# Kernel optimization log

Hardware: AMD Instinct MI355X
Metric: run time of the kernel (lower is better)

The kernel has to match this reference:

```python
import jax, jax.numpy as jnp
import numpy as np

B, C, L = 32, 64, 2048
FREQ = L // 2 + 1            # 1025
BAND_SIZES = [341, 341, 343]  # freq//3, freq//3, remainder


def setup_inputs() -> dict:
    key = jax.random.key(0)
    k = jax.random.split(key, 6)
    X = jax.random.normal(k[0], (B, C, L), dtype=jnp.float32)
    A0 = jax.random.normal(k[1], (BAND_SIZES[0], BAND_SIZES[0]), dtype=jnp.float32)
    A1 = jax.random.normal(k[2], (BAND_SIZES[1], BAND_SIZES[1]), dtype=jnp.float32)
    A2 = jax.random.normal(k[3], (BAND_SIZES[2], BAND_SIZES[2]), dtype=jnp.float32)
    fusion_weights = jnp.ones((3,), dtype=jnp.float32)
    # Gumbel(0,1) noise for the 2-way gumbel-softmax over each (b, i, j) entry
    gumbel_noise = jax.random.gumbel(k[4], (B, C, C, 2), dtype=jnp.float32)
    return {"X": X, "A0": A0, "A1": A1, "A2": A2,
            "fusion_weights": fusion_weights, "gumbel_noise": gumbel_noise}


def _band_dist(band, A):
    # band: (b, c, s), A: (s, s). dist[b,i,j] = ||A (band_i - band_j)||^2
    # Gram trick: ||y_i - y_j||^2 = q_i + q_j - 2 y_i . y_j, y = band @ A^T
    Y = jnp.einsum('ds,bcs->bcd', A, band)          # (b, c, s)
    G = jnp.einsum('bid,bjd->bij', Y, Y)            # (b, c, c)
    q = jnp.einsum('bid,bid->bi', Y, Y)             # (b, c)
    dist = q[:, :, None] + q[:, None, :] - 2.0 * G
    return jnp.maximum(dist, 0.0)                   # guard fp round-off


def reference(X, A0, A1, A2, fusion_weights, gumbel_noise):
    XF = jnp.abs(jnp.fft.rfft(X, axis=-1))          # (b, c, FREQ)
    s0, s1, s2 = BAND_SIZES
    bands = (XF[..., :s0], XF[..., s0:s0 + s1], XF[..., s0 + s1:])
    As = (A0, A1, A2)
    dists = jnp.stack([_band_dist(b_, A_) for b_, A_ in zip(bands, As)], axis=-1)  # (b,c,c,3)
    w = jax.nn.softmax(fusion_weights)
    dist = jnp.einsum('bijk,k->bij', dists, w)      # (b, c, c)

    exp_dist = 1.0 / (dist + 1e-10)
    eye = jnp.eye(C, dtype=exp_dist.dtype)
    mask = 1.0 - eye
    exp_dist = exp_dist * mask
    exp_max = jax.lax.stop_gradient(jnp.max(exp_dist, axis=-1, keepdims=True))
    p = exp_dist / exp_max
    p = (p * mask + eye) * 0.99                     # probs in (0, 0.99]

    # Bernoulli via 2-class gumbel-softmax (hard, tau=1, straight-through)
    logits = jnp.stack([jnp.log(p / (1.0 - p)), jnp.log((1.0 - p) / p)], axis=-1)  # (b,c,c,2)
    y = logits + gumbel_noise
    y_soft = jax.nn.softmax(y, axis=-1)
    y_hard = jax.nn.one_hot(jnp.argmax(y, axis=-1), 2, dtype=y_soft.dtype)
    sample = (y_hard - jax.lax.stop_gradient(y_soft) + y_soft)[..., 0]  # (b,c,c)
    return sample[:, None, :, :]                    # (b, 1, c, c)
```

## Files before the change

kernel.cpp:

```cpp
#include <hip/hip_runtime.h>
#include <math.h>

#define Bn 32
#define Cn 64
#define Ln 2048
#define NFREQ 1025
#define S0c 341
#define S1c 341
#define S2c 343

#define PI_D 3.14159265358979323846

typedef double v4d __attribute__((ext_vector_type(4)));
typedef unsigned short u16;
typedef __attribute__((ext_vector_type(4))) u16 u16x4;
typedef __attribute__((ext_vector_type(8))) short short8;
typedef __attribute__((ext_vector_type(4))) float f32x4;

#define PADIX(i) ((i) + ((i) >> 4))

__device__ __forceinline__ u16 rneb(float f) {
    unsigned u = __float_as_uint(f);
    unsigned r = (u + 0x7FFFu + ((u >> 16) & 1u)) >> 16;
    return (u16)r;
}
__device__ __forceinline__ float b2f(u16 h) {
    return __uint_as_float(((unsigned)h) << 16);
}
__device__ __forceinline__ void split3(float v, u16& h1, u16& h2, u16& h3) {
    h1 = rneb(v);
    float r1 = v - b2f(h1);
    h2 = rneb(r1);
    float r2 = r1 - b2f(h2);
    h3 = rneb(r2);
}

__global__ void k_twiddle(double2* __restrict__ tw) {
    int t = blockIdx.x * blockDim.x + threadIdx.x;
    if (t < 2048) {
        double ang = -2.0 * PI_D * (double)t / 2048.0;
        double s, c;
        sincos(ang, &s, &c);
        tw[t] = make_double2(c, s);
    }
}

__device__ __forceinline__ int rev4_10(unsigned x) {
    unsigned t = __brev(x) >> 22;
    return (int)(((t & 0x155u) << 1) | ((t >> 1) & 0x155u));
}

__global__ __launch_bounds__(256) void k_fft(const float* __restrict__ X,
                                             const double2* __restrict__ tw,
                                             float* __restrict__ XF) {
    __shared__ double re[1088];
    __shared__ double im[1088];
    int row = blockIdx.x;
    int tid = threadIdx.x;
    {
        int k = tid;
        double2 w1 = tw[2 * k];
        double2 w2 = tw[4 * k];
        double2 w3 = tw[6 * k];
        int i0 = PADIX(k), i1 = PADIX(k + 256), i2 = PADIX(k + 512), i3 = PADIX(k + 768);
        const float2* xr = (const float2*)(X + (size_t)row * Ln);
        float2 v0 = xr[k];
        float2 v1 = xr[k + 256];
        float2 v2 = xr[k + 512];
        float2 v3 = xr[k + 768];
        double ar = (double)v0.x, ai = (double)v0.y;
        double br = (double)v1.x, bi = (double)v1.y;
        double cr = (double)v2.x, ci = (double)v2.y;
        double dr = (double)v3.x, di = (double)v3.y;
        double t0r = ar + cr, t0i = ai + ci;
        double t1r = ar - cr, t1i = ai - ci;
        double t2r = br + dr, t2i = bi + di;
        double t3r = br - dr, t3i = bi - di;
        re[i0] = t0r + t2r; im[i0] = t0i + t2i;
        double u1r = t1r + t3i, u1i = t1i - t3r;
        re[i1] = u1r * w1.x - u1i * w1.y; im[i1] = u1r * w1.y + u1i * w1.x;
        double u2r = t0r - t2r, u2i = t0i - t2i;
        re[i2] = u2r * w2.x - u2i * w2.y; im[i2] = u2r * w2.y + u2i * w2.x;
        double u3r = t1r - t3i, u3i = t1i + t3r;
        re[i3] = u3r * w3.x - u3i * w3.y; im[i3] = u3r * w3.y + u3i * w3.x;
    }
    __syncthreads();
    #pragma unroll
    for (int s = 1; s < 5; ++s) {
        int log2Q = 8 - 2 * s;
        int Q = 1 << log2Q;
        int k = tid & (Q - 1);
        int g = tid >> log2Q;
        int base = (g << (log2Q + 2)) + k;
        int i0 = PADIX(base), i1 = PADIX(base + Q), i2 = PADIX(base + 2 * Q), i3 = PADIX(base + 3 * Q);
        int step = 2 << (2 * s);
        double2 w1 = tw[k * step];
        double2 w2 = tw[2 * k * step];
        double2 w3 = tw[3 * k * step];
        double ar = re[i0], ai = im[i0];
        double br = re[i1], bi = im[i1];
        double cr = re[i2], ci = im[i2];
        double dr = re[i3], di = im[i3];
        double t0r = ar + cr, t0i = ai + ci;
        double t1r = ar - cr, t1i = ai - ci;
        double t2r = br + dr, t2i = bi + di;
        double t3r = br - dr, t3i = bi - di;
        re[i0] = t0r + t2r; im[i0] = t0i + t2i;
        double u1r = t1r + t3i, u1i = t1i - t3r;
        re[i1] = u1r * w1.x - u1i * w1.y; im[i1] = u1r * w1.y + u1i * w1.x;
        double u2r = t0r - t2r, u2i = t0i - t2i;
        re[i2] = u2r * w2.x - u2i * w2.y; im[i2] = u2r * w2.y + u2i * w2.x;
        double u3r = t1r - t3i, u3i = t1i + t3r;
        re[i3] = u3r * w3.x - u3i * w3.y; im[i3] = u3r * w3.y + u3i * w3.x;
        __syncthreads();
    }
    float* out0 = XF + (size_t)row * NFREQ;
    for (int k = tid; k <= 1024; k += 256) {
        double Xr, Xi;
        if (k == 0)        { Xr = re[0] + im[0]; Xi = 0.0; }
        else if (k == 1024){ Xr = re[0] - im[0]; Xi = 0.0; }
        else {
            int rv  = PADIX(rev4_10((unsigned)k));
            int rv2 = PADIX(rev4_10((unsigned)(1024 - k)));
            double2 t = tw[k];
            double Zr = re[rv],  Zi = im[rv];
            double Wr = re[rv2], Wi = im[rv2];
            double Er = 0.5 * (Zr + Wr), Ei = 0.5 * (Zi - Wi);
            double Or = 0.5 * (Zi + Wi), Oi = -0.5 * (Zr - Wr);
            Xr = Er + t.x * Or - t.y * Oi;
            Xi = Ei + t.x * Oi + t.y * Or;
        }
        out0[k] = (float)sqrt(Xr * Xr + Xi * Xi);
    }
}

__global__ __launch_bounds__(256) void k_gemm(const float* __restrict__ XF,
                                              const float* __restrict__ A0,
                                              const float* __restrict__ A1,
                                              const float* __restrict__ A2,
                                              double* __restrict__ Y) {
    const int Sarr[3] = {S0c, S1c, S2c};
    const int Oarr[3] = {0, S0c, S0c + S1c};
    int bz = blockIdx.z;
    int z = bz >> 2, q = bz & 3;
    const float* A = (z == 0) ? A0 : ((z == 1) ? A1 : A2);
    int S = Sarr[z], O = Oarr[z];
    int qm = q >> 1, qn = q & 1;

    __shared__ u16 sX1[32][40], sX2[32][40], sX3[32][40];
    __shared__ u16 sA1[32][40], sA2[32][40], sA3[32][40];

    int r0 = blockIdx.x * 64 + qm * 32;
    int d0 = blockIdx.y * 64 + qn * 32;
    int tid = threadIdx.x;
    int lane = tid & 63, w = tid >> 6;
    int lm = (w >> 1) * 16, ln = (w & 1) * 16;
    int fm = lane & 15, kq = lane >> 4;
    int row8 = tid >> 3, seg4 = (tid & 7) * 4;

    f32x4 z4 = {0.0f, 0.0f, 0.0f, 0.0f};
    short8 aone, afm;
    {
        u16 hone = 0x3F80;
        u16 hfm = rneb((float)fm);
        #pragma unroll
        for (int j = 0; j < 8; ++j) { aone[j] = (short)hone; afm[j] = (short)hfm; }
    }
    f32x4 calR = __builtin_amdgcn_mfma_f32_16x16x32_bf16(afm, aone, z4, 0, 0, 0);
    f32x4 calC = __builtin_amdgcn_mfma_f32_16x16x32_bf16(aone, afm, z4, 0, 0, 0);
    int rIdx[4], cIdx[4];
    #pragma unroll
    for (int i = 0; i < 4; ++i) {
        rIdx[i] = (int)(calR[i] * 0.03125f + 0.5f);
        cIdx[i] = (int)(calC[i] * 0.03125f + 0.5f);
    }

    u16x4 wx1, wx2, wx3, wa1, wa2, wa3;
    auto load_tile = [&](int st) {
        int ss0 = st * 32 + seg4;
        const float* xrow = XF + (size_t)(r0 + row8) * NFREQ + O;
        int dA = d0 + row8;
        bool dv = dA < S;
        const float* arow = A + (size_t)dA * S;
        #pragma unroll
        for (int j = 0; j < 4; ++j) {
            int ss = ss0 + j;
            bool sv = ss < S;
            float xv = sv ? xrow[ss] : 0.0f;
            float av = (sv && dv) ? arow[ss] : 0.0f;
            u16 h1, h2, h3;
            split3(xv, h1, h2, h3); wx1[j] = h1; wx2[j] = h2; wx3[j] = h3;
            split3(av, h1, h2, h3); wa1[j] = h1; wa2[j] = h2; wa3[j] = h3;
        }
    };

    double accd[4] = {0.0, 0.0, 0.0, 0.0};
    load_tile(0);
    int nsteps = (S + 31) / 32;
    for (int st = 0; st < nsteps; ++st) {
        __syncthreads();
        *(u16x4*)&sX1[row8][seg4] = wx1;
        *(u16x4*)&sX2[row8][seg4] = wx2;
        *(u16x4*)&sX3[row8][seg4] = wx3;
        *(u16x4*)&sA1[row8][seg4] = wa1;
        *(u16x4*)&sA2[row8][seg4] = wa2;
        *(u16x4*)&sA3[row8][seg4] = wa3;
        __syncthreads();
        if (st + 1 < nsteps) load_tile(st + 1);
        short8 a1 = *(const short8*)&sX1[lm + fm][kq * 8];
        short8 a2 = *(const short8*)&sX2[lm + fm][kq * 8];
        short8 a3 = *(const short8*)&sX3[lm + fm][kq * 8];
        short8 b1 = *(const short8*)&sA1[ln + fm][kq * 8];
        short8 b2 = *(const short8*)&sA2[ln + fm][kq * 8];
        short8 b3 = *(const short8*)&sA3[ln + fm][kq * 8];
        f32x4 p1 = __builtin_amdgcn_mfma_f32_16x16x32_bf16(a1, b1, z4, 0, 0, 0);
        f32x4 p2 = __builtin_amdgcn_mfma_f32_16x16x32_bf16(a1, b2, z4, 0, 0, 0);
        p2 = __builtin_amdgcn_mfma_f32_16x16x32_bf16(a2, b1, p2, 0, 0, 0);
        p2 = __builtin_amdgcn_mfma_f32_16x16x32_bf16(a1, b3, p2, 0, 0, 0);
        p2 = __builtin_amdgcn_mfma_f32_16x16x32_bf16(a2, b2, p2, 0, 0, 0);
        p2 = __builtin_amdgcn_mfma_f32_16x16x32_bf16(a3, b1, p2, 0, 0, 0);
        #pragma unroll
        for (int i = 0; i < 4; ++i)
            accd[i] += (double)p1[i] + (double)p2[i];
    }
    #pragma unroll
    for (int i = 0; i < 4; ++i) {
        int row = r0 + lm + rIdx[i];
        int d = d0 + ln + cIdx[i];
        if (d < S) Y[(size_t)row * NFREQ + O + d] = accd[i];
    }
}

__global__ __launch_bounds__(256) void k_dist(const double* __restrict__ Y,
                                              const float* __restrict__ fw,
                                              double* __restrict__ part) {
    __shared__ double sY[64][34];
    int b = blockIdx.x;
    int chunk = blockIdx.y;
    int dlo = chunk * 128;
    int dhi = (chunk == 7) ? NFREQ : dlo + 128;
    int tid = threadIdx.x;
    int lane = tid & 63, w = tid >> 6;
    int wm = (w >> 1) * 32, wn = (w & 1) * 32;
    int fm = lane & 15, kq = lane >> 4;
    int kl = tid & 31, rl = tid >> 5;

    double f0 = (double)fw[0], f1 = (double)fw[1], f2 = (double)fw[2];
    double m = fmax(f0, fmax(f1, f2));
    double e0 = exp(f0 - m), e1 = exp(f1 - m), e2 = exp(f2 - m);
    double esum = e0 + e1 + e2;
    double sw0 = sqrt(e0 / esum), sw1 = sqrt(e1 / esum), sw2 = sqrt(e2 / esum);

    v4d zero = {0.0, 0.0, 0.0, 0.0};
    double aval = (double)fm;
    v4d calR = __builtin_amdgcn_mfma_f64_16x16x4f64(aval, 1.0, zero, 0, 0, 0);
    v4d calC = __builtin_amdgcn_mfma_f64_16x16x4f64(1.0, aval, zero, 0, 0, 0);
    int rIdx[4], cIdx[4];
    #pragma unroll
    for (int i = 0; i < 4; ++i) {
        rIdx[i] = (int)(calR[i] * 0.25);
        cIdx[i] = (int)(calC[i] * 0.25);
    }

    const double* Yb = Y + (size_t)b * Cn * NFREQ;
    auto load_tile = [&](int k0, double* py) {
        int d = dlo + k0 + kl;
        bool dv = d < dhi;
        double sw = dv ? ((d < S0c) ? sw0 : ((d < S0c + S1c) ? sw1 : sw2)) : 0.0;
        #pragma unroll
        for (int i = 0; i < 8; ++i)
            py[i] = dv ? Yb[(size_t)(rl + 8 * i) * NFREQ + d] * sw : 0.0;
    };

    v4d acc00 = zero, acc01 = zero, acc10 = zero, acc11 = zero;
    double py[8];
    load_tile(0, py);
    int nsteps = (dhi - dlo + 31) / 32;
    for (int st = 0; st < nsteps; ++st) {
        __syncthreads();
        #pragma unroll
        for (int i = 0; i < 8; ++i) sY[rl + 8 * i][kl] = py[i];
        __syncthreads();
        if (st + 1 < nsteps) load_tile((st + 1) * 32, py);
        #pragma unroll
        for (int t = 0; t < 8; ++t) {
            int k = 4 * t + kq;
            double a0 = sY[wm + fm][k];
            double a1 = sY[wm + 16 + fm][k];
            double b0 = sY[wn + fm][k];
            double b1 = sY[wn + 16 + fm][k];
            acc00 = __builtin_amdgcn_mfma_f64_16x16x4f64(a0, b0, acc00, 0, 0, 0);
            acc01 = __builtin_amdgcn_mfma_f64_16x16x4f64(a0, b1, acc01, 0, 0, 0);
            acc10 = __builtin_amdgcn_mfma_f64_16x16x4f64(a1, b0, acc10, 0, 0, 0);
            acc11 = __builtin_amdgcn_mfma_f64_16x16x4f64(a1, b1, acc11, 0, 0, 0);
        }
    }
    double* pb = part + (((size_t)b * 8 + chunk) << 12);
    #pragma unroll
    for (int i = 0; i < 4; ++i) {
        int rowA = wm + rIdx[i], rowB = rowA + 16;
        int cA = wn + cIdx[i], cB = cA + 16;
        pb[rowA * 64 + cA] = acc00[i];
        pb[rowA * 64 + cB] = acc01[i];
        pb[rowB * 64 + cA] = acc10[i];
        pb[rowB * 64 + cB] = acc11[i];
    }
}

__global__ __launch_bounds__(256) void k_decide(const double* __restrict__ part,
                                                const float* __restrict__ gum,
                                                float* __restrict__ out) {
    __shared__ double sQ[64];
    int b = blockIdx.x;
    int tid = threadIdx.x;
    const double* pb = part + (((size_t)b * 8) << 12);
    if (tid < 64) {
        double q = 0.0;
        #pragma unroll
        for (int c = 0; c < 8; ++c) q += pb[((size_t)c << 12) + tid * 65];
        sQ[tid] = q;
    }
    __syncthreads();
    int i = blockIdx.y * 4 + (tid >> 6);
    int j = tid & 63;
    double g = 0.0;
    #pragma unroll
    for (int c = 0; c < 8; ++c) g += pb[((size_t)c << 12) + i * 64 + j];
    double dist = fmax(sQ[i] + sQ[j] - 2.0 * g, 0.0);
    double e = (i == j) ? 0.0 : 1.0 / (dist + 1e-10);
    double emax = e;
    #pragma unroll
    for (int off = 32; off; off >>= 1)
        emax = fmax(emax, __shfl_xor(emax, off, 64));
    double p = (i == j) ? 0.99 : (e / emax) * 0.99;
    double l0 = log(p / (1.0 - p));
    double l1 = -l0;
    int idx = i * 64 + j;
    const float* gb = gum + (size_t)b * 8192;
    double y0 = l0 + (double)gb[2 * idx];
    double y1 = l1 + (double)gb[2 * idx + 1];
    out[(size_t)b * 4096 + idx] = (y0 >= y1) ? 1.0f : 0.0f;
}

extern "C" void kernel_launch(void* const* d_in, const int* in_sizes, int n_in,
                              void* d_out, int out_size, void* d_ws, size_t ws_size,
                              hipStream_t stream) {
    const float* X  = (const float*)d_in[0];
    const float* A0 = (const float*)d_in[1];
    const float* A1 = (const float*)d_in[2];
    const float* A2 = (const float*)d_in[3];
    const float* fw = (const float*)d_in[4];
    const float* gm = (const float*)d_in[5];
    float* out = (float*)d_out;

    char* ws = (char*)d_ws;
    double2* tw  = (double2*)(ws);
    float*   XF  = (float*)(ws + 32768);
    double*  Y   = (double*)(ws + 8429568);
    double*  part = (double*)(ws + 32768);

    k_twiddle<<<8, 256, 0, stream>>>(tw);
    k_fft<<<Bn * Cn, 256, 0, stream>>>(X, tw, XF);
    k_gemm<<<dim3(32, 6, 12), 256, 0, stream>>>(XF, A0, A1, A2, Y);
    k_dist<<<dim3(Bn, 8), 256, 0, stream>>>(Y, fw, part);
    k_decide<<<dim3(Bn, 16), 256, 0, stream>>>(part, gm, out);
}
```

Measured before the change: 160.3 us.

## Pre-split operands into padded bf16 planes before GEMM instead of inside tile loads

Moves the three-way bf16 split of the spectrum into the FFT epilogue and the split of the A matrices into a prep kernel that also computes the twiddles. Both are written as zero-padded 352-wide planes, so the GEMM tile loader becomes plain vector u16x4 loads with no bounds checks and no per-tile split arithmetic. Previously each GEMM block redid the split for every tile it touched. In exchange it adds workspace traffic for three u16 planes and a larger prep launch, and every band now runs a fixed 11 K-steps.

```diff
diff --git a/kernel.cpp b/kernel.cpp
--- a/kernel.cpp
+++ b/kernel.cpp
@@ -8,6 +8,9 @@
 #define S0c 341
 #define S1c 341
 #define S2c 343
+#define KPAD 352
+#define XROW (3 * 1056)
+#define APLANE (3 * KPAD * KPAD)
 
 #define PI_D 3.14159265358979323846
 
@@ -35,24 +38,44 @@
     h3 = rneb(r2);
 }
 
-__global__ void k_twiddle(double2* __restrict__ tw) {
-    int t = blockIdx.x * blockDim.x + threadIdx.x;
-    if (t < 2048) {
+__device__ __forceinline__ int rev4_10(unsigned x) {
+    unsigned t = __brev(x) >> 22;
+    return (int)(((t & 0x155u) << 1) | ((t >> 1) & 0x155u));
+}
+
+__global__ __launch_bounds__(256) void k_prep(const float* __restrict__ A0,
+                                              const float* __restrict__ A1,
+                                              const float* __restrict__ A2,
+                                              double2* __restrict__ tw,
+                                              u16* __restrict__ AS) {
+    int b = blockIdx.x;
+    int tid = threadIdx.x;
+    if (b < 8) {
+        int t = b * 256 + tid;
         double ang = -2.0 * PI_D * (double)t / 2048.0;
         double s, c;
         sincos(ang, &s, &c);
         tw[t] = make_double2(c, s);
-    }
-}
-
-__device__ __forceinline__ int rev4_10(unsigned x) {
-    unsigned t = __brev(x) >> 22;
-    return (int)(((t & 0x155u) << 1) | ((t >> 1) & 0x155u));
+        return;
+    }
+    int i = b - 8;
+    int z = i / 484;
+    const float* A = (z == 0) ? A0 : ((z == 1) ? A1 : A2);
+    int S = (z == 2) ? S2c : S0c;
+    int idx = (i % 484) * 256 + tid;
+    int d = idx / KPAD, kk = idx - d * KPAD;
+    float v = (d < S && kk < S) ? A[(size_t)d * S + kk] : 0.0f;
+    u16 h1, h2, h3;
+    split3(v, h1, h2, h3);
+    size_t o = ((size_t)z * KPAD + d) * KPAD + kk;
+    AS[o] = h1;
+    AS[APLANE + o] = h2;
+    AS[2 * (size_t)APLANE + o] = h3;
 }
 
 __global__ __launch_bounds__(256) void k_fft(const float* __restrict__ X,
                                              const double2* __restrict__ tw,
-                                             float* __restrict__ XF) {
+                                             u16* __restrict__ XS) {
     __shared__ double re[1088];
     __shared__ double im[1088];
     int row = blockIdx.x;
@@ -114,7 +137,11 @@
         re[i3] = u3r * w3.x - u3i * w3.y; im[i3] = u3r * w3.y + u3i * w3.x;
         __syncthreads();
     }
-    float* out0 = XF + (size_t)row * NFREQ;
+    u16* xrow = XS + (size_t)row * XROW;
+    if (tid < 31) {
+        int pp = (tid < 11) ? (341 + tid) : ((tid < 22) ? (682 + tid) : (1025 + tid));
+        xrow[pp] = 0; xrow[1056 + pp] = 0; xrow[2112 + pp] = 0;
+    }
     for (int k = tid; k <= 1024; k += 256) {
         double Xr, Xi;
         if (k == 0)        { Xr = re[0] + im[0]; Xi = 0.0; }
@@ -130,20 +157,24 @@
             Xr = Er + t.x * Or - t.y * Oi;
             Xi = Ei + t.x * Oi + t.y * Or;
         }
-        out0[k] = (float)sqrt(Xr * Xr + Xi * Xi);
-    }
-}
-
-__global__ __launch_bounds__(256) void k_gemm(const float* __restrict__ XF,
-                                              const float* __restrict__ A0,
-                                              const float* __restrict__ A1,
-                                              const float* __restrict__ A2,
+        float v = (float)sqrt(Xr * Xr + Xi * Xi);
+        int zb = (k < S0c) ? 0 : ((k < S0c + S1c) ? 1 : 2);
+        int pos = k + 11 * zb;
+        u16 h1, h2, h3;
+        split3(v, h1, h2, h3);
+        xrow[pos] = h1;
+        xrow[1056 + pos] = h2;
+        xrow[2112 + pos] = h3;
+    }
+}
+
+__global__ __launch_bounds__(256) void k_gemm(const u16* __restrict__ XS,
+                                              const u16* __restrict__ AS,
                                               double* __restrict__ Y) {
     const int Sarr[3] = {S0c, S1c, S2c};
     const int Oarr[3] = {0, S0c, S0c + S1c};
     int bz = blockIdx.z;
     int z = bz >> 2, q = bz & 3;
-    const float* A = (z == 0) ? A0 : ((z == 1) ? A1 : A2);
     int S = Sarr[z], O = Oarr[z];
     int qm = q >> 1, qn = q & 1;
 
@@ -175,28 +206,23 @@
         cIdx[i] = (int)(calC[i] * 0.03125f + 0.5f);
     }
 
+    const u16* xbase = XS + (size_t)(r0 + row8) * XROW + (size_t)z * KPAD + seg4;
+    const u16* abase = AS + ((size_t)z * KPAD + (d0 + row8)) * KPAD + seg4;
+
     u16x4 wx1, wx2, wx3, wa1, wa2, wa3;
     auto load_tile = [&](int st) {
-        int ss0 = st * 32 + seg4;
-        const float* xrow = XF + (size_t)(r0 + row8) * NFREQ + O;
-        int dA = d0 + row8;
-        bool dv = dA < S;
-        const float* arow = A + (size_t)dA * S;
-        #pragma unroll
-        for (int j = 0; j < 4; ++j) {
-            int ss = ss0 + j;
-            bool sv = ss < S;
-            float xv = sv ? xrow[ss] : 0.0f;
-            float av = (sv && dv) ? arow[ss] : 0.0f;
-            u16 h1, h2, h3;
-            split3(xv, h1, h2, h3); wx1[j] = h1; wx2[j] = h2; wx3[j] = h3;
-            split3(av, h1, h2, h3); wa1[j] = h1; wa2[j] = h2; wa3[j] = h3;
-        }
+        int ko = st * 32;
+        wx1 = *(const u16x4*)(xbase + ko);
+        wx2 = *(const u16x4*)(xbase + 1056 + ko);
+        wx3 = *(const u16x4*)(xbase + 2112 + ko);
+        wa1 = *(const u16x4*)(abase + ko);
+        wa2 = *(const u16x4*)(abase + APLANE + ko);
+        wa3 = *(const u16x4*)(abase + 2 * (size_t)APLANE + ko);
     };
 
     double accd[4] = {0.0, 0.0, 0.0, 0.0};
     load_tile(0);
-    int nsteps = (S + 31) / 32;
+    const int nsteps = KPAD / 32;
     for (int st = 0; st < nsteps; ++st) {
         __syncthreads();
         *(u16x4*)&sX1[row8][seg4] = wx1;
@@ -354,14 +380,15 @@
     float* out = (float*)d_out;
 
     char* ws = (char*)d_ws;
-    double2* tw  = (double2*)(ws);
-    float*   XF  = (float*)(ws + 32768);
-    double*  Y   = (double*)(ws + 8429568);
-    double*  part = (double*)(ws + 32768);
-
-    k_twiddle<<<8, 256, 0, stream>>>(tw);
-    k_fft<<<Bn * Cn, 256, 0, stream>>>(X, tw, XF);
-    k_gemm<<<dim3(32, 6, 12), 256, 0, stream>>>(XF, A0, A1, A2, Y);
+    double2* tw = (double2*)(ws);
+    u16*  XS = (u16*)(ws + 32768);
+    u16*  AS = (u16*)(ws + 13008896);
+    double* Y = (double*)(ws + 15239168);
+    double* part = (double*)(ws + 32768);
+
+    k_prep<<<1460, 256, 0, stream>>>(A0, A1, A2, tw, AS);
+    k_fft<<<Bn * Cn, 256, 0, stream>>>(X, tw, XS);
+    k_gemm<<<dim3(32, 6, 12), 256, 0, stream>>>(XS, AS, Y);
     k_dist<<<dim3(Bn, 8), 256, 0, stream>>>(Y, fw, part);
     k_decide<<<dim3(Bn, 16), 256, 0, stream>>>(part, gm, out);
 }
```

After: 146.5 us. 8.6% less time.
